# Optimization experiments

Hardware: AMD Instinct MI355X
Metric: run time of the kernel (lower is better)

The kernel has to match this reference:

```python
import jax, jax.numpy as jnp
import numpy as np

B, TQ, TK, DQ, DK, DV = 16, 1024, 1024, 1024, 1024, 1024


def setup_inputs() -> dict:
    key = jax.random.key(0)
    k1, k2, k3, k4, k5 = jax.random.split(key, 5)
    query = jax.random.normal(k1, (B, TQ, DQ), dtype=jnp.float32)
    keys = jax.random.normal(k2, (B, TK, DK), dtype=jnp.float32)
    values = jax.random.normal(k3, (B, TK, DV), dtype=jnp.float32)
    W = jax.random.normal(k4, (DQ, DK), dtype=jnp.float32) / np.sqrt(DQ)
    mask = jax.random.normal(k5, (B, TK), dtype=jnp.float32)
    return {"query": query, "keys": keys, "values": values, "W": W, "mask": mask}


def reference(query, keys, values, W, mask):
    # Bilinear (Luong 'general') score: weight[b,q,k] = query[b,q,:] @ W @ keys[b,k,:]
    qW = jnp.einsum('bqd,de->bqe', query, W)              # [B, Tq, Dk]
    weight = jnp.einsum('bqe,bke->bqk', qW, keys)         # [B, Tq, Tk]
    weight = weight + mask[:, None, :]                    # additive mask, broadcast over Tq
    score = jax.nn.softmax(weight, axis=-1)               # [B, Tq, Tk]
    ctx = jnp.einsum('bqk,bkv->bqv', score, values)       # [B, Tq, Dv]
    return (score, ctx)
```

## Files before the change

### kernel.cpp

```cpp
#include <hip/hip_runtime.h>
#include <hip/hip_bf16.h>

typedef _Float16 f16;
typedef __attribute__((ext_vector_type(8))) _Float16 half8;
typedef __attribute__((ext_vector_type(4))) float f32x4;

#define BM 256
#define BN 256
#define BK 64

__device__ __forceinline__ void gl2lds16(const f16* g, const f16* l) {
    __builtin_amdgcn_global_load_lds(
        (const __attribute__((address_space(1))) unsigned int*)g,
        (__attribute__((address_space(3))) unsigned int*)l, 16, 0, 0);
}

#define MFMA(d, a, b) d = __builtin_amdgcn_mfma_f32_16x16x32_f16(a, b, d, 0, 0, 0)

__global__ __launch_bounds__(256)
void cast_f16(const float* __restrict__ in, f16* __restrict__ out, long long n) {
    long long i = ((long long)blockIdx.x * 256 + threadIdx.x) * 8;
    if (i >= n) return;
    float4 a = *(const float4*)&in[i];
    float4 b = *(const float4*)&in[i + 4];
    union { f16 h[8]; uint4 q; } H;
    H.h[0] = (f16)a.x; H.h[1] = (f16)a.y; H.h[2] = (f16)a.z; H.h[3] = (f16)a.w;
    H.h[4] = (f16)b.x; H.h[5] = (f16)b.y; H.h[6] = (f16)b.z; H.h[7] = (f16)b.w;
    *(uint4*)&out[i] = H.q;
}

__global__ __launch_bounds__(256)
void transpose64_f16(const float* __restrict__ in, f16* __restrict__ out,
                     int R, int C, long long in_stride, long long out_stride) {
    const int b = blockIdx.z;
    in += (size_t)b * in_stride;
    out += (size_t)b * out_stride;

    __shared__ float tile[64][68];
    const int c0 = blockIdx.x * 64, r0 = blockIdx.y * 64;
    const int t = threadIdx.x;

    const int lr = t >> 4, lc4 = (t & 15) * 4;
#pragma unroll
    for (int p = 0; p < 4; p++) {
        float4 v = *(const float4*)&in[(size_t)(r0 + p * 16 + lr) * C + c0 + lc4];
        *(float4*)&tile[p * 16 + lr][lc4] = v;
    }
    __syncthreads();

    const int oc_ = t >> 3, rr = (t & 7) * 8;
#pragma unroll
    for (int p = 0; p < 2; p++) {
        const int oc = p * 32 + oc_;
        union { f16 h[8]; uint4 q; } H;
#pragma unroll
        for (int i = 0; i < 8; i++) H.h[i] = (f16)tile[rr + i][oc];
        *(uint4*)&out[(size_t)(c0 + oc) * R + r0 + rr] = H.q;
    }
}

template<int EPI, int XR>
__global__ __launch_bounds__(512, 2)
void gemm256(const f16* __restrict__ A_, const f16* __restrict__ B_,
             float* __restrict__ Cf, f16* __restrict__ Ch,
             int M, int N, int K,
             long long batchA, long long batchB, long long batchC) {
    int bx, by, bz;
    if constexpr (XR == 1) {
        const int d = blockIdx.z * 16 + blockIdx.y * 4 + blockIdx.x;
        const int xcd = d & 7, j = d >> 3, i2 = j & 15;
        bz = xcd + 8 * (j >> 4); by = i2 >> 2; bx = i2 & 3;
    } else {
        bx = blockIdx.x; by = blockIdx.y; bz = blockIdx.z;
    }
    const int b = bz;
    const int m0 = by * BM;
    const int n0 = bx * BN;
    const int t = threadIdx.x;
    const int lane = t & 63, wv = t >> 6;
    const int wr = wv >> 2;
    const int wc = wv & 3;

    const f16* A = A_ + (size_t)b * batchA;
    const f16* B = B_ + (size_t)b * batchB;

    __shared__ alignas(16) f16 sA[2][2][128][64];
    __shared__ alignas(16) f16 sB[2][2][128][64];

    const int srow  = wv * 16 + (lane >> 3);
    const int gslot = (lane & 7) ^ (lane >> 3);

    const f16* gAl  = A + (size_t)(m0 + srow) * K + gslot * 8;
    const f16* gAl8 = gAl + (size_t)8 * K;
    const f16* gAh  = gAl + (size_t)128 * K;
    const f16* gAh8 = gAl8 + (size_t)128 * K;
    const f16* gBl  = B + (size_t)(n0 + srow) * K + gslot * 8;
    const f16* gBl8 = gBl + (size_t)8 * K;
    const f16* gBh  = gBl + (size_t)128 * K;
    const f16* gBh8 = gBl8 + (size_t)128 * K;

    f32x4 acc[8][4];
#pragma unroll
    for (int i = 0; i < 8; i++)
#pragma unroll
        for (int j = 0; j < 4; j++)
#pragma unroll
            for (int r = 0; r < 4; r++) acc[i][j][r] = 0.0f;

    gl2lds16(gAl,  &sA[0][0][wv * 16][0]); gl2lds16(gAl8, &sA[0][0][wv * 16 + 8][0]);
    gl2lds16(gAh,  &sA[0][1][wv * 16][0]); gl2lds16(gAh8, &sA[0][1][wv * 16 + 8][0]);
    gl2lds16(gBl,  &sB[0][0][wv * 16][0]); gl2lds16(gBl8, &sB[0][0][wv * 16 + 8][0]);
    gl2lds16(gBh,  &sB[0][1][wv * 16][0]); gl2lds16(gBh8, &sB[0][1][wv * 16 + 8][0]);

    const int fr  = lane & 15;
    const int fq4 = lane >> 4;
    const int NT  = K / BK;

    half8 af[4][2], bA[2][2], bB[2][2];

    for (int tt = 0; tt < NT; ++tt) {
        const int c = tt & 1, cn = c ^ 1;
        const size_t kg = (size_t)(tt + 1) * BK;
        const bool nx = (tt + 1 < NT);

        const f16* pa = &sA[c][wr][fr][0];
        const f16* pb = &sB[c][wc >> 1][(wc & 1) * 64 + fr][0];
        const int cs0 = ((0 + fq4) ^ (fr & 7)) * 8;
        const int cs1 = ((4 + fq4) ^ (fr & 7)) * 8;

        if (nx) {
            gl2lds16(gAl + kg,  &sA[cn][0][wv * 16][0]);
            gl2lds16(gAl8 + kg, &sA[cn][0][wv * 16 + 8][0]);
            asm volatile("s_waitcnt vmcnt(2)\n\ts_barrier" ::: "memory");
        } else {
            asm volatile("s_waitcnt vmcnt(0)\n\ts_barrier" ::: "memory");
        }
#pragma unroll
        for (int mi = 0; mi < 4; mi++) {
            af[mi][0] = *(const half8*)(pa + mi * 1024 + cs0);
            af[mi][1] = *(const half8*)(pa + mi * 1024 + cs1);
        }
#pragma unroll
        for (int ni = 0; ni < 2; ni++) {
            bA[ni][0] = *(const half8*)(pb + ni * 1024 + cs0);
            bA[ni][1] = *(const half8*)(pb + ni * 1024 + cs1);
        }
#pragma unroll
        for (int ni = 0; ni < 2; ni++) {
            bB[ni][0] = *(const half8*)(pb + (2 + ni) * 1024 + cs0);
            bB[ni][1] = *(const half8*)(pb + (2 + ni) * 1024 + cs1);
        }
        __builtin_amdgcn_s_setprio(1);
#pragma unroll
        for (int mi = 0; mi < 4; mi++)
#pragma unroll
            for (int ni = 0; ni < 2; ni++) {
                MFMA(acc[mi][ni], af[mi][0], bA[ni][0]);
                MFMA(acc[mi][ni], af[mi][1], bA[ni][1]);
            }
        __builtin_amdgcn_s_setprio(0);

        if (nx) {
            gl2lds16(gAh + kg,  &sA[cn][1][wv * 16][0]);
            gl2lds16(gAh8 + kg, &sA[cn][1][wv * 16 + 8][0]);
        }
        __builtin_amdgcn_s_setprio(1);
#pragma unroll
        for (int mi = 0; mi < 4; mi++)
#pragma unroll
            for (int ni = 0; ni < 2; ni++) {
                MFMA(acc[mi][2 + ni], af[mi][0], bB[ni][0]);
                MFMA(acc[mi][2 + ni], af[mi][1], bB[ni][1]);
            }
        __builtin_amdgcn_s_setprio(0);

        if (nx) {
            gl2lds16(gBl + kg,  &sB[cn][0][wv * 16][0]);
            gl2lds16(gBl8 + kg, &sB[cn][0][wv * 16 + 8][0]);
        }
#pragma unroll
        for (int mi = 0; mi < 4; mi++) {
            af[mi][0] = *(const half8*)(pa + (64 + mi * 16) * 64 + cs0);
            af[mi][1] = *(const half8*)(pa + (64 + mi * 16) * 64 + cs1);
        }
        __builtin_amdgcn_s_setprio(1);
#pragma unroll
        for (int mi = 0; mi < 4; mi++)
#pragma unroll
            for (int ni = 0; ni < 2; ni++) {
                MFMA(acc[4 + mi][2 + ni], af[mi][0], bB[ni][0]);
                MFMA(acc[4 + mi][2 + ni], af[mi][1], bB[ni][1]);
            }
        __builtin_amdgcn_s_setprio(0);

        if (nx) {
            gl2lds16(gBh + kg,  &sB[cn][1][wv * 16][0]);
            gl2lds16(gBh8 + kg, &sB[cn][1][wv * 16 + 8][0]);
        }
        __builtin_amdgcn_s_setprio(1);
#pragma unroll
        for (int mi = 0; mi < 4; mi++)
#pragma unroll
            for (int ni = 0; ni < 2; ni++) {
                MFMA(acc[4 + mi][ni], af[mi][0], bA[ni][0]);
                MFMA(acc[4 + mi][ni], af[mi][1], bA[ni][1]);
            }
        __builtin_amdgcn_s_setprio(0);
        asm volatile("s_barrier" ::: "memory");
    }

    const int q4 = (lane >> 4) * 4;
#pragma unroll
    for (int mi = 0; mi < 8; mi++)
#pragma unroll
        for (int ni = 0; ni < 4; ni++) {
            const int col = n0 + wc * 64 + ni * 16 + fr;
#pragma unroll
            for (int r = 0; r < 4; r++) {
                const int row = m0 + wr * 128 + mi * 16 + q4 + r;
                const size_t idx = (size_t)b * batchC + (size_t)row * N + col;
                float v = acc[mi][ni][r];
                if constexpr (EPI == 0) Cf[idx] = v;
                else                    Ch[idx] = (f16)v;
            }
        }
}

__global__ __launch_bounds__(512, 2)
void gemm_softmax(const f16* __restrict__ A_, const f16* __restrict__ B_,
                  const float* __restrict__ mask,
                  float* __restrict__ score, f16* __restrict__ sc,
                  int N, int K, long long MAT) {
    const int d = blockIdx.z * 16 + blockIdx.y;
    const int xcd = d & 7, j = d >> 3;
    const int b = xcd + 8 * (j >> 4);
    const int m0 = (j & 15) * 64;

    const int t = threadIdx.x;
    const int lane = t & 63, wv = t >> 6;
    const int fr = lane & 15;

    const f16* A = A_ + (size_t)b * MAT;
    const f16* B = B_ + (size_t)b * MAT;

    __shared__ alignas(16) f16 sA2[2][64][32];
    __shared__ alignas(16) f16 sB2[2][1024][32];
    __shared__ float sRed[8][64];
    __shared__ float sRed2[64];

    const int brow = lane >> 2;
    const int gsl  = (lane & 3) ^ ((lane >> 2) & 3);
    const f16* gB = B + (size_t)(wv * 128 + brow) * K + gsl * 8;
    const f16* gA = A + (size_t)(m0 + wv * 8 + brow) * K + gsl * 8;

    f32x4 acc[4][8];
#pragma unroll
    for (int mi = 0; mi < 4; mi++)
#pragma unroll
        for (int ni = 0; ni < 8; ni++)
#pragma unroll
            for (int r = 0; r < 4; r++) acc[mi][ni][r] = 0.0f;

#pragma unroll
    for (int i = 0; i < 8; i++)
        gl2lds16(gB + (size_t)i * 16 * K, &sB2[0][wv * 128 + i * 16][0]);
    if (lane < 32) gl2lds16(gA, &sA2[0][wv * 8][0]);

    const int NT = K / 32;
    half8 afr[4], bfr[8];

    for (int tt = 0; tt < NT; ++tt) {
        const int c = tt & 1, cn = c ^ 1;
        const size_t kg = (size_t)(tt + 1) * 32;
        const bool nx = (tt + 1 < NT);

        if (nx) {
#pragma unroll
            for (int i = 0; i < 8; i++)
                gl2lds16(gB + (size_t)i * 16 * K + kg, &sB2[cn][wv * 128 + i * 16][0]);
            if (lane < 32) gl2lds16(gA + kg, &sA2[cn][wv * 8][0]);
            asm volatile("s_waitcnt vmcnt(9)\n\ts_barrier" ::: "memory");
        } else {
            asm volatile("s_waitcnt vmcnt(0)\n\ts_barrier" ::: "memory");
        }

        const int sl = ((lane >> 4) ^ (fr & 3)) * 8;
#pragma unroll
        for (int mi = 0; mi < 4; mi++)
            afr[mi] = *(const half8*)&sA2[c][mi * 16 + fr][sl];
#pragma unroll
        for (int ni = 0; ni < 8; ni++)
            bfr[ni] = *(const half8*)&sB2[c][wv * 128 + ni * 16 + fr][sl];

        __builtin_amdgcn_s_setprio(1);
#pragma unroll
        for (int ni = 0; ni < 8; ni++)
#pragma unroll
            for (int mi = 0; mi < 4; mi++)
                MFMA(acc[mi][ni], afr[mi], bfr[ni]);
        __builtin_amdgcn_s_setprio(0);

        asm volatile("s_barrier" ::: "memory");
    }

    const int q4 = (lane >> 4) * 4;

    float mv[8];
#pragma unroll
    for (int ni = 0; ni < 8; ni++)
        mv[ni] = mask[(size_t)b * N + wv * 128 + ni * 16 + fr];
#pragma unroll
    for (int mi = 0; mi < 4; mi++)
#pragma unroll
        for (int ni = 0; ni < 8; ni++)
#pragma unroll
            for (int r = 0; r < 4; r++) acc[mi][ni][r] += mv[ni];

    float pm[4][4];
#pragma unroll
    for (int mi = 0; mi < 4; mi++)
#pragma unroll
        for (int r = 0; r < 4; r++) {
            float x = acc[mi][0][r];
#pragma unroll
            for (int ni = 1; ni < 8; ni++) x = fmaxf(x, acc[mi][ni][r]);
            pm[mi][r] = x;
        }
#pragma unroll
    for (int o = 1; o < 16; o <<= 1)
#pragma unroll
        for (int mi = 0; mi < 4; mi++)
#pragma unroll
            for (int r = 0; r < 4; r++)
                pm[mi][r] = fmaxf(pm[mi][r], __shfl_xor(pm[mi][r], o));

    if (fr == 0)
#pragma unroll
        for (int mi = 0; mi < 4; mi++)
#pragma unroll
            for (int r = 0; r < 4; r++)
                sRed[wv][mi * 16 + q4 + r] = pm[mi][r];
    __syncthreads();
    if (t < 64) {
        float x = sRed[0][t];
#pragma unroll
        for (int w = 1; w < 8; w++) x = fmaxf(x, sRed[w][t]);
        sRed2[t] = x;
    }
    __syncthreads();

    float m_[4][4];
#pragma unroll
    for (int mi = 0; mi < 4; mi++)
#pragma unroll
        for (int r = 0; r < 4; r++) m_[mi][r] = sRed2[mi * 16 + q4 + r];

    float ps[4][4];
#pragma unroll
    for (int mi = 0; mi < 4; mi++)
#pragma unroll
        for (int r = 0; r < 4; r++) ps[mi][r] = 0.0f;
#pragma unroll
    for (int mi = 0; mi < 4; mi++)
#pragma unroll
        for (int ni = 0; ni < 8; ni++)
#pragma unroll
            for (int r = 0; r < 4; r++) {
                float e = __expf(acc[mi][ni][r] - m_[mi][r]);
                acc[mi][ni][r] = e;
                ps[mi][r] += e;
            }
#pragma unroll
    for (int o = 1; o < 16; o <<= 1)
#pragma unroll
        for (int mi = 0; mi < 4; mi++)
#pragma unroll
            for (int r = 0; r < 4; r++)
                ps[mi][r] += __shfl_xor(ps[mi][r], o);

    if (fr == 0)
#pragma unroll
        for (int mi = 0; mi < 4; mi++)
#pragma unroll
            for (int r = 0; r < 4; r++)
                sRed[wv][mi * 16 + q4 + r] = ps[mi][r];
    __syncthreads();
    if (t < 64) {
        float x = sRed[0][t];
#pragma unroll
        for (int w = 1; w < 8; w++) x += sRed[w][t];
        sRed2[t] = x;
    }
    __syncthreads();

    float inv[4][4];
#pragma unroll
    for (int mi = 0; mi < 4; mi++)
#pragma unroll
        for (int r = 0; r < 4; r++) inv[mi][r] = 1.0f / sRed2[mi * 16 + q4 + r];

#pragma unroll
    for (int mi = 0; mi < 4; mi++)
#pragma unroll
        for (int ni = 0; ni < 8; ni++) {
            const int col = wv * 128 + ni * 16 + fr;
#pragma unroll
            for (int r = 0; r < 4; r++) {
                const int row = m0 + mi * 16 + q4 + r;
                const size_t idx = (size_t)b * MAT + (size_t)row * N + col;
                float v = acc[mi][ni][r] * inv[mi][r];
                score[idx] = v;
                sc[idx] = (f16)v;
            }
        }
}

extern "C" void kernel_launch(void* const* d_in, const int* in_sizes, int n_in,
                              void* d_out, int out_size, void* d_ws, size_t ws_size,
                              hipStream_t stream) {
    const int B = 16, T = 1024, D = 1024;
    const long long MAT = (long long)T * D;
    const long long BT = (long long)B * MAT;

    const float* query  = (const float*)d_in[0];
    const float* keys   = (const float*)d_in[1];
    const float* values = (const float*)d_in[2];
    const float* W      = (const float*)d_in[3];
    const float* mask   = (const float*)d_in[4];

    float* out = (float*)d_out;
    float* score_f = out;
    float* ctx_f   = out + (size_t)BT;

    char* ws = (char*)d_ws;
    f16* R1  = (f16*)ws;                   ws += (size_t)BT * 2;
    f16* R2  = (f16*)ws;                   ws += (size_t)BT * 2;
    f16* R3  = (f16*)ws;                   ws += (size_t)BT * 2;
    f16* wt  = (f16*)ws;                   ws += (size_t)MAT * 2;

    f16* qf = R1, *sc = R1;
    f16* kf = R2;
    f16* qw = R3, *vt = R3;

    dim3 blk(256);
    dim3 blk5(512);

    cast_f16<<<dim3((unsigned)(BT / 2048)), blk, 0, stream>>>(query, qf, BT);
    transpose64_f16<<<dim3(16, 16, 1), blk, 0, stream>>>(W, wt, D, D, 0, 0);

    gemm256<2, 0><<<dim3(4, 64, 1), blk5, 0, stream>>>(
        qf, wt, nullptr, qw, B * T, D, D, 0, 0, 0);

    cast_f16<<<dim3((unsigned)(BT / 2048)), blk, 0, stream>>>(keys, kf, BT);

    gemm_softmax<<<dim3(1, 16, B), blk5, 0, stream>>>(
        qw, kf, mask, score_f, sc, T, D, MAT);

    transpose64_f16<<<dim3(16, 16, B), blk, 0, stream>>>(values, vt, T, D, MAT, MAT);

    gemm256<0, 1><<<dim3(4, 4, B), blk5, 0, stream>>>(
        sc, vt, ctx_f, nullptr, T, D, T, MAT, MAT, MAT);
}
```

Measured before the change: 421.8 us.

## Restructure GEMM prefetch pipelines and fuse query/key casts into one launch

The gemm256 main loop now waits for all loads and barriers once per iteration, then issues the A and B prefetches in two groups instead of four interleaved ones, and drops the trailing barrier. The gemm_softmax loop is split into four sub-steps, each issuing two B-row prefetches with finer vmcnt waits, and the LDS swizzle gains an extra XOR term to reduce bank conflicts. The query and key f16 casts are merged into one two-row grid launch, removing a kernel launch. The tighter waits and the removed barrier risk races or stalls if vmcnt counts do not match the number of loads in flight.

```diff
diff --git a/kernel.cpp b/kernel.cpp
--- a/kernel.cpp
+++ b/kernel.cpp
@@ -15,10 +15,18 @@
         (__attribute__((address_space(3))) unsigned int*)l, 16, 0, 0);
 }
 
+template<int V>
+__device__ __forceinline__ void waitv() {
+    asm volatile("s_waitcnt vmcnt(%0)" :: "i"(V) : "memory");
+}
+
 #define MFMA(d, a, b) d = __builtin_amdgcn_mfma_f32_16x16x32_f16(a, b, d, 0, 0, 0)
 
 __global__ __launch_bounds__(256)
-void cast_f16(const float* __restrict__ in, f16* __restrict__ out, long long n) {
+void cast2_f16(const float* __restrict__ in0, f16* __restrict__ out0,
+               const float* __restrict__ in1, f16* __restrict__ out1, long long n) {
+    const float* in = blockIdx.y ? in1 : in0;
+    f16* out       = blockIdx.y ? out1 : out0;
     long long i = ((long long)blockIdx.x * 256 + threadIdx.x) * 8;
     if (i >= n) return;
     float4 a = *(const float4*)&in[i];
@@ -128,12 +136,13 @@
         const int cs0 = ((0 + fq4) ^ (fr & 7)) * 8;
         const int cs1 = ((4 + fq4) ^ (fr & 7)) * 8;
 
+        asm volatile("s_waitcnt vmcnt(0)\n\ts_barrier" ::: "memory");
+
         if (nx) {
             gl2lds16(gAl + kg,  &sA[cn][0][wv * 16][0]);
             gl2lds16(gAl8 + kg, &sA[cn][0][wv * 16 + 8][0]);
-            asm volatile("s_waitcnt vmcnt(2)\n\ts_barrier" ::: "memory");
-        } else {
-            asm volatile("s_waitcnt vmcnt(0)\n\ts_barrier" ::: "memory");
+            gl2lds16(gAh + kg,  &sA[cn][1][wv * 16][0]);
+            gl2lds16(gAh8 + kg, &sA[cn][1][wv * 16 + 8][0]);
         }
 #pragma unroll
         for (int mi = 0; mi < 4; mi++) {
@@ -161,8 +170,10 @@
         __builtin_amdgcn_s_setprio(0);
 
         if (nx) {
-            gl2lds16(gAh + kg,  &sA[cn][1][wv * 16][0]);
-            gl2lds16(gAh8 + kg, &sA[cn][1][wv * 16 + 8][0]);
+            gl2lds16(gBl + kg,  &sB[cn][0][wv * 16][0]);
+            gl2lds16(gBl8 + kg, &sB[cn][0][wv * 16 + 8][0]);
+            gl2lds16(gBh + kg,  &sB[cn][1][wv * 16][0]);
+            gl2lds16(gBh8 + kg, &sB[cn][1][wv * 16 + 8][0]);
         }
         __builtin_amdgcn_s_setprio(1);
 #pragma unroll
@@ -174,10 +185,6 @@
             }
         __builtin_amdgcn_s_setprio(0);
 
-        if (nx) {
-            gl2lds16(gBl + kg,  &sB[cn][0][wv * 16][0]);
-            gl2lds16(gBl8 + kg, &sB[cn][0][wv * 16 + 8][0]);
-        }
 #pragma unroll
         for (int mi = 0; mi < 4; mi++) {
             af[mi][0] = *(const half8*)(pa + (64 + mi * 16) * 64 + cs0);
@@ -193,10 +200,6 @@
             }
         __builtin_amdgcn_s_setprio(0);
 
-        if (nx) {
-            gl2lds16(gBh + kg,  &sB[cn][1][wv * 16][0]);
-            gl2lds16(gBh8 + kg, &sB[cn][1][wv * 16 + 8][0]);
-        }
         __builtin_amdgcn_s_setprio(1);
 #pragma unroll
         for (int mi = 0; mi < 4; mi++)
@@ -206,7 +209,6 @@
                 MFMA(acc[4 + mi][ni], af[mi][1], bA[ni][1]);
             }
         __builtin_amdgcn_s_setprio(0);
-        asm volatile("s_barrier" ::: "memory");
     }
 
     const int q4 = (lane >> 4) * 4;
@@ -238,7 +240,7 @@
 
     const int t = threadIdx.x;
     const int lane = t & 63, wv = t >> 6;
-    const int fr = lane & 15;
+    const int fr = lane & 15, fq4 = lane >> 4;
 
     const f16* A = A_ + (size_t)b * MAT;
     const f16* B = B_ + (size_t)b * MAT;
@@ -248,10 +250,13 @@
     __shared__ float sRed[8][64];
     __shared__ float sRed2[64];
 
-    const int brow = lane >> 2;
-    const int gsl  = (lane & 3) ^ ((lane >> 2) & 3);
-    const f16* gB = B + (size_t)(wv * 128 + brow) * K + gsl * 8;
-    const f16* gA = A + (size_t)(m0 + wv * 8 + brow) * K + gsl * 8;
+    const int gslB = ((lane & 3) ^ ((lane >> 2) & 3) ^ (lane >> 4)) & 3;
+    const int gslA = ((lane & 3) ^ ((lane >> 2) & 3) ^ ((wv * 2 + (lane >> 4)) & 3)) & 3;
+    const f16* gB = B + (size_t)(wv * 128 + (lane >> 2)) * K + gslB * 8;
+    const f16* gA = A + (size_t)(m0 + wv * 8 + (lane >> 2)) * K + gslA * 8;
+
+#define STB(cn_, i_, kg_) gl2lds16(gB + (size_t)(i_) * 16 * K + (kg_), &sB2[cn_][wv * 128 + (i_) * 16][0])
+#define STA(cn_, kg_)     if (lane < 32) gl2lds16(gA + (kg_), &sA2[cn_][wv * 8][0])
 
     f32x4 acc[4][8];
 #pragma unroll
@@ -261,12 +266,12 @@
 #pragma unroll
             for (int r = 0; r < 4; r++) acc[mi][ni][r] = 0.0f;
 
-#pragma unroll
-    for (int i = 0; i < 8; i++)
-        gl2lds16(gB + (size_t)i * 16 * K, &sB2[0][wv * 128 + i * 16][0]);
-    if (lane < 32) gl2lds16(gA, &sA2[0][wv * 8][0]);
+    STB(0, 0, 0); STB(0, 1, 0); STA(0, 0);
+#pragma unroll
+    for (int i = 2; i < 8; i++) STB(0, i, 0);
 
     const int NT = K / 32;
+    const int sl = ((fq4 ^ (fr & 3) ^ (fr >> 2)) & 3) * 8;
     half8 afr[4], bfr[8];
 
     for (int tt = 0; tt < NT; ++tt) {
@@ -274,34 +279,48 @@
         const size_t kg = (size_t)(tt + 1) * 32;
         const bool nx = (tt + 1 < NT);
 
-        if (nx) {
-#pragma unroll
-            for (int i = 0; i < 8; i++)
-                gl2lds16(gB + (size_t)i * 16 * K + kg, &sB2[cn][wv * 128 + i * 16][0]);
-            if (lane < 32) gl2lds16(gA + kg, &sA2[cn][wv * 8][0]);
-            asm volatile("s_waitcnt vmcnt(9)\n\ts_barrier" ::: "memory");
-        } else {
-            asm volatile("s_waitcnt vmcnt(0)\n\ts_barrier" ::: "memory");
-        }
-
-        const int sl = ((lane >> 4) ^ (fr & 3)) * 8;
+        waitv<6>();
+        asm volatile("s_barrier" ::: "memory");
+        if (nx) { STB(cn, 0, kg); STB(cn, 1, kg); STA(cn, kg); }
 #pragma unroll
         for (int mi = 0; mi < 4; mi++)
             afr[mi] = *(const half8*)&sA2[c][mi * 16 + fr][sl];
-#pragma unroll
-        for (int ni = 0; ni < 8; ni++)
-            bfr[ni] = *(const half8*)&sB2[c][wv * 128 + ni * 16 + fr][sl];
-
-        __builtin_amdgcn_s_setprio(1);
-#pragma unroll
-        for (int ni = 0; ni < 8; ni++)
-#pragma unroll
-            for (int mi = 0; mi < 4; mi++)
-                MFMA(acc[mi][ni], afr[mi], bfr[ni]);
-        __builtin_amdgcn_s_setprio(0);
-
-        asm volatile("s_barrier" ::: "memory");
-    }
+        bfr[0] = *(const half8*)&sB2[c][wv * 128 + 0 * 16 + fr][sl];
+        bfr[1] = *(const half8*)&sB2[c][wv * 128 + 1 * 16 + fr][sl];
+        __builtin_amdgcn_s_setprio(1);
+#pragma unroll
+        for (int mi = 0; mi < 4; mi++) { MFMA(acc[mi][0], afr[mi], bfr[0]); MFMA(acc[mi][1], afr[mi], bfr[1]); }
+        __builtin_amdgcn_s_setprio(0);
+
+        if (nx) waitv<7>(); else waitv<4>();
+        if (nx) { STB(cn, 2, kg); STB(cn, 3, kg); }
+        bfr[2] = *(const half8*)&sB2[c][wv * 128 + 2 * 16 + fr][sl];
+        bfr[3] = *(const half8*)&sB2[c][wv * 128 + 3 * 16 + fr][sl];
+        __builtin_amdgcn_s_setprio(1);
+#pragma unroll
+        for (int mi = 0; mi < 4; mi++) { MFMA(acc[mi][2], afr[mi], bfr[2]); MFMA(acc[mi][3], afr[mi], bfr[3]); }
+        __builtin_amdgcn_s_setprio(0);
+
+        if (nx) waitv<7>(); else waitv<2>();
+        if (nx) { STB(cn, 4, kg); STB(cn, 5, kg); }
+        bfr[4] = *(const half8*)&sB2[c][wv * 128 + 4 * 16 + fr][sl];
+        bfr[5] = *(const half8*)&sB2[c][wv * 128 + 5 * 16 + fr][sl];
+        __builtin_amdgcn_s_setprio(1);
+#pragma unroll
+        for (int mi = 0; mi < 4; mi++) { MFMA(acc[mi][4], afr[mi], bfr[4]); MFMA(acc[mi][5], afr[mi], bfr[5]); }
+        __builtin_amdgcn_s_setprio(0);
+
+        if (nx) waitv<7>(); else waitv<0>();
+        if (nx) { STB(cn, 6, kg); STB(cn, 7, kg); }
+        bfr[6] = *(const half8*)&sB2[c][wv * 128 + 6 * 16 + fr][sl];
+        bfr[7] = *(const half8*)&sB2[c][wv * 128 + 7 * 16 + fr][sl];
+        __builtin_amdgcn_s_setprio(1);
+#pragma unroll
+        for (int mi = 0; mi < 4; mi++) { MFMA(acc[mi][6], afr[mi], bfr[6]); MFMA(acc[mi][7], afr[mi], bfr[7]); }
+        __builtin_amdgcn_s_setprio(0);
+    }
+#undef STB
+#undef STA
 
     const int q4 = (lane >> 4) * 4;
 
@@ -445,14 +464,12 @@
     dim3 blk(256);
     dim3 blk5(512);
 
-    cast_f16<<<dim3((unsigned)(BT / 2048)), blk, 0, stream>>>(query, qf, BT);
+    cast2_f16<<<dim3((unsigned)(BT / 2048), 2), blk, 0, stream>>>(query, qf, keys, kf, BT);
     transpose64_f16<<<dim3(16, 16, 1), blk, 0, stream>>>(W, wt, D, D, 0, 0);
 
     gemm256<2, 0><<<dim3(4, 64, 1), blk5, 0, stream>>>(
         qf, wt, nullptr, qw, B * T, D, D, 0, 0, 0);
 
-    cast_f16<<<dim3((unsigned)(BT / 2048)), blk, 0, stream>>>(keys, kf, BT);
-
     gemm_softmax<<<dim3(1, 16, B), blk5, 0, stream>>>(
         qw, kf, mask, score_f, sc, T, D, MAT);
 
```

Result: no change. 423.2 us (+0.3%).
